# Kernel tuning notes

Hardware: AMD Instinct MI355X
Metric: run time of the kernel (lower is better)

Reference implementation:

```python
import jax, jax.numpy as jnp
import numpy as np

N = 50000      # nodes
IN = 256       # in_feat
H = 4          # num_heads
DH = 64        # out_feat // num_heads
R = 6          # number of relations
E = 300000     # edges per relation
NEG_SLOPE = 0.2  # DGL GATConv leaky_relu slope


def setup_inputs() -> dict:
    key = jax.random.key(0)
    ks = jax.random.split(key, 7)
    x = jax.random.normal(ks[0], (N, IN), dtype=jnp.float32)
    W = jax.random.normal(ks[1], (R, IN, H * DH), dtype=jnp.float32) * (1.0 / np.sqrt(IN))
    attn_l = jax.random.normal(ks[2], (R, H, DH), dtype=jnp.float32) * 0.1
    attn_r = jax.random.normal(ks[3], (R, H, DH), dtype=jnp.float32) * 0.1
    bias = jax.random.normal(ks[4], (R, H * DH), dtype=jnp.float32) * 0.01
    src = jax.random.randint(ks[5], (R, E), 0, N, dtype=jnp.int32).astype(jnp.int64)
    dst = jax.random.randint(ks[6], (R, E), 0, N, dtype=jnp.int32).astype(jnp.int64)
    return {"x": x, "W": W, "attn_l": attn_l, "attn_r": attn_r, "bias": bias,
            "src": src, "dst": dst}


def reference(x, W, attn_l, attn_r, bias, src, dst):
    n = x.shape[0]
    r_total, h, dh = attn_l.shape
    out = jnp.zeros((n, h, dh), dtype=x.dtype)
    # small fixed loop over structurally-distinct relations (HeteroGraphConv)
    for r in range(r_total):
        feat = (x @ W[r]).reshape(n, h, dh)            # [N,H,Dh] shared src/dst proj
        el = jnp.sum(feat * attn_l[r], axis=-1)        # [N,H]
        er = jnp.sum(feat * attn_r[r], axis=-1)        # [N,H]
        s, d = src[r], dst[r]
        e = jax.nn.leaky_relu(el[s] + er[d], NEG_SLOPE)  # [E,H]
        # segmented softmax over incoming edges of each dst node
        m = jax.ops.segment_max(e, d, num_segments=n)    # [N,H]
        m = jnp.where(jnp.isfinite(m), m, 0.0)
        a = jnp.exp(e - m[d])                            # [E,H]
        z = jax.ops.segment_sum(a, d, num_segments=n)    # [N,H]
        alpha = a / jnp.maximum(z[d], 1e-9)              # [E,H]
        msg = alpha[:, :, None] * feat[s]                # [E,H,Dh]
        agg = jax.ops.segment_sum(msg, d, num_segments=n)  # [N,H,Dh]
        # GATConv: bias + activation(relu) per relation, HeteroGraphConv sums
        out = out + jax.nn.relu(agg + bias[r].reshape(h, dh))
    hcat = out.reshape(n, h * dh)                        # merge='cat' view
    return jax.nn.relu(hcat)                             # layer-level activation
```

## Files before the change

### kernel.cpp

```cpp
#include <hip/hip_runtime.h>

#define NN 50000
#define MP 50048
#define NH 4
#define NR 6
#define NE 300000
#define HD 256
#define SLOTS 32
#define NB 512
#define BSZ ((NE + NB - 1) / NB)

typedef __attribute__((ext_vector_type(4))) float f32x4;
typedef __attribute__((ext_vector_type(8))) short bf16x8;

__device__ __forceinline__ short f2bf(float f) {
  unsigned u = __float_as_uint(f);
  unsigned r = (u + 0x7FFFu + ((u >> 16) & 1u)) >> 16;
  return (short)r;
}
__device__ __forceinline__ float bf2f_lo(unsigned d) {
  return __uint_as_float(d << 16);
}
__device__ __forceinline__ float bf2f_hi(unsigned d) {
  return __uint_as_float(d & 0xffff0000u);
}

#define GLOAD_LDS16(g, l)                                                     \
  __builtin_amdgcn_global_load_lds(                                           \
      (const __attribute__((address_space(1))) void*)(g),                     \
      (__attribute__((address_space(3))) void*)(l), 16, 0, 0)

__global__ __launch_bounds__(256) void cast_x_kernel(
    const float* __restrict__ x, short* __restrict__ xb, int n4) {
  const int i = blockIdx.x * 256 + threadIdx.x;
  if (i >= n4) return;
  const float4 v = ((const float4*)x)[i];
  short4 o;
  o.x = f2bf(v.x); o.y = f2bf(v.y); o.z = f2bf(v.z); o.w = f2bf(v.w);
  ((short4*)xb)[i] = o;
}

__global__ __launch_bounds__(256) void cast_wt_kernel(
    const float* __restrict__ W, short* __restrict__ wt) {
  const int o = blockIdx.x * 256 + threadIdx.x;
  if (o >= NR * 256 * 256) return;
  const int r = o >> 16;
  const int nrow = (o >> 8) & 255;
  const int k = o & 255;
  wt[o] = f2bf(W[r * 65536 + k * 256 + nrow]);
}

__global__ __launch_bounds__(256) void gemm_kernel(
    const short* __restrict__ xb,
    const short* __restrict__ wt_all,
    const float* __restrict__ attn_l,
    const float* __restrict__ attn_r,
    short* __restrict__ featb_all,
    float* __restrict__ el_all, float* __restrict__ er_all) {
  __shared__ short As[128 * 32];
  __shared__ short Bs[128 * 32];
  const int t = threadIdx.x;
  const int lane = t & 63;
  const int w = t >> 6;
  const int wm = w & 1, wn = w >> 1;
  const int row0 = blockIdx.x * 128;
  const int n0 = blockIdx.y * 128;
  const int r = blockIdx.z;
  const short* wt = wt_all + (size_t)r * 65536;
  short* featb = featb_all + (size_t)r * MP * 256;

  f32x4 acc[4][4];
#pragma unroll
  for (int mi = 0; mi < 4; ++mi)
#pragma unroll
    for (int ni = 0; ni < 4; ++ni) {
      f32x4 z = {0.f, 0.f, 0.f, 0.f};
      acc[mi][ni] = z;
    }

  const int c0 = t, c1 = 256 + t;
  int ar0 = row0 + (c0 >> 2); if (ar0 >= NN) ar0 = NN - 1;
  int ar1 = row0 + (c1 >> 2); if (ar1 >= NN) ar1 = NN - 1;
  const short* ag0 = xb + (size_t)ar0 * 256 + (c0 & 3) * 8;
  const short* ag1 = xb + (size_t)ar1 * 256 + (c1 & 3) * 8;
  const short* bg0 = wt + (size_t)(n0 + (c0 >> 2)) * 256 + (c0 & 3) * 8;
  const short* bg1 = wt + (size_t)(n0 + (c1 >> 2)) * 256 + (c1 & 3) * 8;
  short* la0 = As + c0 * 8;
  short* la1 = As + c1 * 8;
  short* lb0 = Bs + c0 * 8;
  short* lb1 = Bs + c1 * 8;

  const int ra = lane & 15;
  const int qa = (lane >> 4) * 8;

  for (int k0 = 0; k0 < 256; k0 += 32) {
    GLOAD_LDS16(ag0 + k0, la0);
    GLOAD_LDS16(ag1 + k0, la1);
    GLOAD_LDS16(bg0 + k0, lb0);
    GLOAD_LDS16(bg1 + k0, lb1);
    __syncthreads();
    bf16x8 af[4], bfr[4];
#pragma unroll
    for (int mi = 0; mi < 4; ++mi)
      af[mi] = *(const bf16x8*)&As[(wm * 64 + mi * 16 + ra) * 32 + qa];
#pragma unroll
    for (int ni = 0; ni < 4; ++ni)
      bfr[ni] = *(const bf16x8*)&Bs[(wn * 64 + ni * 16 + ra) * 32 + qa];
#pragma unroll
    for (int mi = 0; mi < 4; ++mi)
#pragma unroll
      for (int ni = 0; ni < 4; ++ni)
        acc[mi][ni] = __builtin_amdgcn_mfma_f32_16x16x32_bf16(
            af[mi], bfr[ni], acc[mi][ni], 0, 0, 0);
    __syncthreads();
  }

  const int h = (n0 >> 6) + wn;
  float alv[4], arv[4];
#pragma unroll
  for (int ni = 0; ni < 4; ++ni) {
    alv[ni] = attn_l[r * HD + h * 64 + ni * 16 + ra];
    arv[ni] = attn_r[r * HD + h * 64 + ni * 16 + ra];
  }
#pragma unroll
  for (int mi = 0; mi < 4; ++mi) {
#pragma unroll
    for (int j = 0; j < 4; ++j) {
      const int row = row0 + wm * 64 + mi * 16 + (lane >> 4) * 4 + j;
      float elp = 0.f, erp = 0.f;
#pragma unroll
      for (int ni = 0; ni < 4; ++ni) {
        const float v = acc[mi][ni][j];
        featb[(size_t)row * 256 + n0 + wn * 64 + ni * 16 + ra] = f2bf(v);
        elp = fmaf(v, alv[ni], elp);
        erp = fmaf(v, arv[ni], erp);
      }
#pragma unroll
      for (int m = 1; m < 16; m <<= 1) {
        elp += __shfl_xor(elp, m, 64);
        erp += __shfl_xor(erp, m, 64);
      }
      if (ra == 0 && row < NN) {
        el_all[((size_t)r * NN + row) * NH + h] = elp;
        er_all[((size_t)r * NN + row) * NH + h] = erp;
      }
    }
  }
}

__global__ __launch_bounds__(256) void build_kernel(
    const int* __restrict__ src, const int* __restrict__ dst,
    int* __restrict__ deg, unsigned short* __restrict__ slots) {
  const int lo = blockIdx.x * BSZ;
  const int hi = (lo + BSZ < NE) ? lo + BSZ : NE;
  for (int r = 0; r < NR; ++r) {
    for (int i = lo + threadIdx.x; i < hi; i += 256) {
      const int s = src[(size_t)r * NE + i];
      const int d = dst[(size_t)r * NE + i];
      const int g = r * NN + d;
      const int sl = atomicAdd(&deg[g], 1);
      if (sl < SLOTS)
        slots[(size_t)g * SLOTS + sl] = (unsigned short)s;
    }
  }
}

__global__ __launch_bounds__(256) void agg_kernel(
    const short* __restrict__ featb_all, const float* __restrict__ el_all,
    const float* __restrict__ er_all, const int* __restrict__ deg,
    const unsigned short* __restrict__ slots, const float* __restrict__ bias,
    float* __restrict__ out) {
  const int wid = (blockIdx.x * 256 + threadIdx.x) >> 6;
  const int lane = threadIdx.x & 63;
  if (wid >= NN) return;
  const int h = lane >> 4;
  const int c0 = lane * 4;

  float oacc[4] = {0.f, 0.f, 0.f, 0.f};
  const int wid_u = __builtin_amdgcn_readfirstlane(wid);

  {
    const int g = (NR - 1) * NN + wid_u;
    (void)g;
  }
  const int g_first = (NR - 1) * NN + wid_u;
  const uint4* spf = (const uint4*)(slots + (size_t)g_first * SLOTS);
  uint4 sq0 = spf[0], sq1 = spf[1], sq2 = spf[2], sq3 = spf[3];
  int dgv = deg[g_first];
  float erv = er_all[(size_t)g_first * NH + h];

  for (int r = NR - 1; r >= 0; --r) {
    const int dg0 = __builtin_amdgcn_readfirstlane(dgv);
    const int dg = dg0 > SLOTS ? SLOTS : dg0;
    unsigned sdv[16];
    sdv[0]  = __builtin_amdgcn_readfirstlane(sq0.x);
    sdv[1]  = __builtin_amdgcn_readfirstlane(sq0.y);
    sdv[2]  = __builtin_amdgcn_readfirstlane(sq0.z);
    sdv[3]  = __builtin_amdgcn_readfirstlane(sq0.w);
    sdv[4]  = __builtin_amdgcn_readfirstlane(sq1.x);
    sdv[5]  = __builtin_amdgcn_readfirstlane(sq1.y);
    sdv[6]  = __builtin_amdgcn_readfirstlane(sq1.z);
    sdv[7]  = __builtin_amdgcn_readfirstlane(sq1.w);
    sdv[8]  = __builtin_amdgcn_readfirstlane(sq2.x);
    sdv[9]  = __builtin_amdgcn_readfirstlane(sq2.y);
    sdv[10] = __builtin_amdgcn_readfirstlane(sq2.z);
    sdv[11] = __builtin_amdgcn_readfirstlane(sq2.w);
    sdv[12] = __builtin_amdgcn_readfirstlane(sq3.x);
    sdv[13] = __builtin_amdgcn_readfirstlane(sq3.y);
    sdv[14] = __builtin_amdgcn_readfirstlane(sq3.z);
    sdv[15] = __builtin_amdgcn_readfirstlane(sq3.w);
    const float er_nh = erv;

    if (r > 0) {
      const int g2 = (r - 1) * NN + wid_u;
      const uint4* sp2 = (const uint4*)(slots + (size_t)g2 * SLOTS);
      sq0 = sp2[0]; sq1 = sp2[1]; sq2 = sp2[2]; sq3 = sp2[3];
      dgv = deg[g2];
      erv = er_all[(size_t)g2 * NH + h];
    }

    const float* elr = el_all + (size_t)r * NN * NH;
    const short* fb = featb_all + (size_t)r * MP * 256;

    float z = 0.f;
    float acc[4] = {0.f, 0.f, 0.f, 0.f};

#pragma unroll
    for (int j0 = 0; j0 < SLOTS; j0 += 8) {
      if (j0 >= dg) break;
      float pv[8];
      uint2 rw[8];
#pragma unroll
      for (int k = 0; k < 8; ++k) {
        const int e = j0 + k;
        int s = (int)((e & 1) ? (sdv[e >> 1] >> 16) : (sdv[e >> 1] & 0xffffu));
        const bool v = e < dg;
        s = v ? s : 0;
        rw[k] = *(const uint2*)(fb + (size_t)s * 256 + c0);
        float ev = elr[s * NH + h] + er_nh;
        ev = fmaxf(ev, 0.2f * ev);
        pv[k] = v ? __expf(ev) : 0.f;
      }
#pragma unroll
      for (int k = 0; k < 8; ++k) {
        z += pv[k];
        acc[0] = fmaf(pv[k], bf2f_lo(rw[k].x), acc[0]);
        acc[1] = fmaf(pv[k], bf2f_hi(rw[k].x), acc[1]);
        acc[2] = fmaf(pv[k], bf2f_lo(rw[k].y), acc[2]);
        acc[3] = fmaf(pv[k], bf2f_hi(rw[k].y), acc[3]);
      }
    }

    const float inv = 1.f / fmaxf(z, 1e-9f);
    const float4 bv = *(const float4*)(bias + r * HD + c0);
    oacc[0] += fmaxf(fmaf(acc[0], inv, bv.x), 0.f);
    oacc[1] += fmaxf(fmaf(acc[1], inv, bv.y), 0.f);
    oacc[2] += fmaxf(fmaf(acc[2], inv, bv.z), 0.f);
    oacc[3] += fmaxf(fmaf(acc[3], inv, bv.w), 0.f);
  }

  float4 o4 = {oacc[0], oacc[1], oacc[2], oacc[3]};
  *(float4*)(out + (size_t)wid * 256 + c0) = o4;
}

extern "C" void kernel_launch(void* const* d_in, const int* in_sizes, int n_in,
                              void* d_out, int out_size, void* d_ws,
                              size_t ws_size, hipStream_t stream) {
  const float* x      = (const float*)d_in[0];
  const float* W      = (const float*)d_in[1];
  const float* attn_l = (const float*)d_in[2];
  const float* attn_r = (const float*)d_in[3];
  const float* bias   = (const float*)d_in[4];
  const int*   src    = (const int*)d_in[5];
  const int*   dst    = (const int*)d_in[6];
  float* out = (float*)d_out;

  char* p = (char*)d_ws;
  auto alloc = [&](size_t bytes) {
    char* r = p;
    p += (bytes + 255) & ~(size_t)255;
    return r;
  };
  short* xb    = (short*)alloc((size_t)NN * HD * 2);
  short* wt    = (short*)alloc((size_t)NR * 256 * 256 * 2);
  short* featb = (short*)alloc((size_t)NR * MP * 256 * 2);
  float* el    = (float*)alloc((size_t)NR * NN * NH * 4);
  float* er    = (float*)alloc((size_t)NR * NN * NH * 4);
  int*   deg   = (int*)alloc((size_t)NR * NN * 4);
  unsigned short* slots =
      (unsigned short*)alloc((size_t)NR * NN * SLOTS * 2);

  hipMemsetAsync(deg, 0, (size_t)NR * NN * 4, stream);

  cast_x_kernel<<<(NN * HD / 4 + 255) / 256, 256, 0, stream>>>(x, xb,
                                                               NN * HD / 4);
  cast_wt_kernel<<<(NR * 256 * 256 + 255) / 256, 256, 0, stream>>>(W, wt);
  build_kernel<<<NB, 256, 0, stream>>>(src, dst, deg, slots);
  gemm_kernel<<<dim3(MP / 128, 2, NR), 256, 0, stream>>>(xb, wt, attn_l,
                                                         attn_r, featb, el,
                                                         er);
  agg_kernel<<<(NN * 64) / 256, 256, 0, stream>>>(featb, el, er, deg, slots,
                                                  bias, out);
}
```

Before: 473.3 us.

## Deepen GEMM K-tile to 64 with XOR-swizzled LDS and tile the W transpose

```diff
diff --git a/kernel.cpp b/kernel.cpp
--- a/kernel.cpp
+++ b/kernel.cpp
@@ -42,12 +42,26 @@
 
 __global__ __launch_bounds__(256) void cast_wt_kernel(
     const float* __restrict__ W, short* __restrict__ wt) {
-  const int o = blockIdx.x * 256 + threadIdx.x;
-  if (o >= NR * 256 * 256) return;
-  const int r = o >> 16;
-  const int nrow = (o >> 8) & 255;
-  const int k = o & 255;
-  wt[o] = f2bf(W[r * 65536 + k * 256 + nrow]);
+  __shared__ float ts[32][33];
+  const int bx = blockIdx.x;
+  const int r = bx >> 6;
+  const int tile = bx & 63;
+  const int k0 = (tile >> 3) * 32;
+  const int n0 = (tile & 7) * 32;
+  const int t = threadIdx.x;
+  const int col = t & 31;
+  const int rr = t >> 5;
+#pragma unroll
+  for (int p = 0; p < 4; ++p) {
+    const int row = p * 8 + rr;
+    ts[row][col] = W[(size_t)r * 65536 + (k0 + row) * 256 + n0 + col];
+  }
+  __syncthreads();
+#pragma unroll
+  for (int p = 0; p < 4; ++p) {
+    const int row = p * 8 + rr;
+    wt[(size_t)r * 65536 + (n0 + row) * 256 + k0 + col] = f2bf(ts[col][row]);
+  }
 }
 
 __global__ __launch_bounds__(256) void gemm_kernel(
@@ -57,8 +71,8 @@
     const float* __restrict__ attn_r,
     short* __restrict__ featb_all,
     float* __restrict__ el_all, float* __restrict__ er_all) {
-  __shared__ short As[128 * 32];
-  __shared__ short Bs[128 * 32];
+  __shared__ short As[128 * 64];
+  __shared__ short Bs[128 * 64];
   const int t = threadIdx.x;
   const int lane = t & 63;
   const int w = t >> 6;
@@ -78,40 +92,54 @@
       acc[mi][ni] = z;
     }
 
-  const int c0 = t, c1 = 256 + t;
-  int ar0 = row0 + (c0 >> 2); if (ar0 >= NN) ar0 = NN - 1;
-  int ar1 = row0 + (c1 >> 2); if (ar1 >= NN) ar1 = NN - 1;
-  const short* ag0 = xb + (size_t)ar0 * 256 + (c0 & 3) * 8;
-  const short* ag1 = xb + (size_t)ar1 * 256 + (c1 & 3) * 8;
-  const short* bg0 = wt + (size_t)(n0 + (c0 >> 2)) * 256 + (c0 & 3) * 8;
-  const short* bg1 = wt + (size_t)(n0 + (c1 >> 2)) * 256 + (c1 & 3) * 8;
-  short* la0 = As + c0 * 8;
-  short* la1 = As + c1 * 8;
-  short* lb0 = Bs + c0 * 8;
-  short* lb1 = Bs + c1 * 8;
+  const short* ag[4];
+  const short* bg[4];
+  short* la[4];
+  short* lb[4];
+#pragma unroll
+  for (int i = 0; i < 4; ++i) {
+    const int c = t + 256 * i;
+    const int row = c >> 3;
+    const int sslot = (c & 7) ^ (row & 7);
+    int ar = row0 + row; if (ar >= NN) ar = NN - 1;
+    ag[i] = xb + (size_t)ar * 256 + sslot * 8;
+    bg[i] = wt + (size_t)(n0 + row) * 256 + sslot * 8;
+    la[i] = As + c * 8;
+    lb[i] = Bs + c * 8;
+  }
 
   const int ra = lane & 15;
-  const int qa = (lane >> 4) * 8;
-
-  for (int k0 = 0; k0 < 256; k0 += 32) {
-    GLOAD_LDS16(ag0 + k0, la0);
-    GLOAD_LDS16(ag1 + k0, la1);
-    GLOAD_LDS16(bg0 + k0, lb0);
-    GLOAD_LDS16(bg1 + k0, lb1);
+  const int qg = lane >> 4;
+
+  for (int k0 = 0; k0 < 256; k0 += 64) {
+#pragma unroll
+    for (int i = 0; i < 4; ++i) {
+      GLOAD_LDS16(ag[i] + k0, la[i]);
+      GLOAD_LDS16(bg[i] + k0, lb[i]);
+    }
     __syncthreads();
-    bf16x8 af[4], bfr[4];
-#pragma unroll
-    for (int mi = 0; mi < 4; ++mi)
-      af[mi] = *(const bf16x8*)&As[(wm * 64 + mi * 16 + ra) * 32 + qa];
-#pragma unroll
-    for (int ni = 0; ni < 4; ++ni)
-      bfr[ni] = *(const bf16x8*)&Bs[(wn * 64 + ni * 16 + ra) * 32 + qa];
-#pragma unroll
-    for (int mi = 0; mi < 4; ++mi)
-#pragma unroll
-      for (int ni = 0; ni < 4; ++ni)
-        acc[mi][ni] = __builtin_amdgcn_mfma_f32_16x16x32_bf16(
-            af[mi], bfr[ni], acc[mi][ni], 0, 0, 0);
+#pragma unroll
+    for (int kk = 0; kk < 2; ++kk) {
+      bf16x8 af[4], bfr[4];
+#pragma unroll
+      for (int mi = 0; mi < 4; ++mi) {
+        const int rw = wm * 64 + mi * 16 + ra;
+        const int ch = (kk * 4 + qg) ^ (rw & 7);
+        af[mi] = *(const bf16x8*)&As[rw * 64 + ch * 8];
+      }
+#pragma unroll
+      for (int ni = 0; ni < 4; ++ni) {
+        const int rw = wn * 64 + ni * 16 + ra;
+        const int ch = (kk * 4 + qg) ^ (rw & 7);
+        bfr[ni] = *(const bf16x8*)&Bs[rw * 64 + ch * 8];
+      }
+#pragma unroll
+      for (int mi = 0; mi < 4; ++mi)
+#pragma unroll
+        for (int ni = 0; ni < 4; ++ni)
+          acc[mi][ni] = __builtin_amdgcn_mfma_f32_16x16x32_bf16(
+              af[mi], bfr[ni], acc[mi][ni], 0, 0, 0);
+    }
     __syncthreads();
   }
 
@@ -179,10 +207,6 @@
   float oacc[4] = {0.f, 0.f, 0.f, 0.f};
   const int wid_u = __builtin_amdgcn_readfirstlane(wid);
 
-  {
-    const int g = (NR - 1) * NN + wid_u;
-    (void)g;
-  }
   const int g_first = (NR - 1) * NN + wid_u;
   const uint4* spf = (const uint4*)(slots + (size_t)g_first * SLOTS);
   uint4 sq0 = spf[0], sq1 = spf[1], sq2 = spf[2], sq3 = spf[3];
@@ -294,7 +318,7 @@
 
   cast_x_kernel<<<(NN * HD / 4 + 255) / 256, 256, 0, stream>>>(x, xb,
                                                                NN * HD / 4);
-  cast_wt_kernel<<<(NR * 256 * 256 + 255) / 256, 256, 0, stream>>>(W, wt);
+  cast_wt_kernel<<<NR * 64, 256, 0, stream>>>(W, wt);
   build_kernel<<<NB, 256, 0, stream>>>(src, dst, deg, slots);
   gemm_kernel<<<dim3(MP / 128, 2, NR), 256, 0, stream>>>(xb, wt, attn_l,
                                                          attn_r, featb, el,
```

New measurement: 466.0 us. Within noise of the previous version (-1.5%).
